# Optimization experiments

Hardware: AMD Instinct MI355X
Metric: run time of the kernel (lower is better)

The kernel has to match this reference:

```python
import jax, jax.numpy as jnp
import numpy as np

N = 250000
E = 8000000
G = 1024  # num graphs
F_IN = 16
H = 9
EPS_BN = 1e-5


def gat_conv(x, edge_index, W, att_src, att_dst, bias):
    # PyG GATConv (heads=1, add_self_loops=True, negative_slope=0.2)
    h = x @ W                               # [N, H]
    src = jnp.concatenate([edge_index[0], jnp.arange(N)])  # self-loops
    dst = jnp.concatenate([edge_index[1], jnp.arange(N)])
    a_src = h @ att_src                     # [N]
    a_dst = h @ att_dst                     # [N]
    e = jax.nn.leaky_relu(a_src[src] + a_dst[dst], 0.2)    # [E+N]
    m = jax.lax.stop_gradient(jax.ops.segment_max(e, dst, num_segments=N))
    ex = jnp.exp(e - m[dst])
    s = jax.ops.segment_sum(ex, dst, num_segments=N)
    alpha = ex / (s[dst] + 1e-16)
    out = jax.ops.segment_sum(h[src] * alpha[:, None], dst, num_segments=N)
    return out + bias


def batch_norm(x, gamma, beta):
    mu = x.mean(0)
    var = x.var(0)  # biased, as PyTorch uses for normalization
    return gamma * (x - mu) * jax.lax.rsqrt(var + EPS_BN) + beta


def setup_inputs() -> dict:
    key = jax.random.key(0)
    ks = jax.random.split(key, 20)
    x = jax.random.normal(ks[0], (N, F_IN), dtype=jnp.float32)
    edge_index = jax.random.randint(ks[1], (2, E), 0, N, dtype=jnp.int64)
    batch = jnp.sort(jax.random.randint(ks[2], (N,), 0, G, dtype=jnp.int64))
    p = {}
    p['W1'] = jax.random.normal(ks[3], (F_IN, H), dtype=jnp.float32) * 0.3
    p['as1'] = jax.random.normal(ks[4], (H,), dtype=jnp.float32) * 0.3
    p['ad1'] = jax.random.normal(ks[5], (H,), dtype=jnp.float32) * 0.3
    p['b1'] = jnp.zeros((H,), dtype=jnp.float32)
    p['g1'] = jnp.ones((H,), dtype=jnp.float32)
    p['be1'] = jnp.zeros((H,), dtype=jnp.float32)
    p['W2'] = jax.random.normal(ks[6], (H, H), dtype=jnp.float32) * 0.3
    p['as2'] = jax.random.normal(ks[7], (H,), dtype=jnp.float32) * 0.3
    p['ad2'] = jax.random.normal(ks[8], (H,), dtype=jnp.float32) * 0.3
    p['b2'] = jnp.zeros((H,), dtype=jnp.float32)
    p['g2'] = jnp.ones((H,), dtype=jnp.float32)
    p['be2'] = jnp.zeros((H,), dtype=jnp.float32)
    for i, (di, do) in enumerate([(H, H), (H, H), (H, H), (H, 1)], start=1):
        p[f'mW{i}'] = jax.random.normal(ks[8 + 2 * i], (di, do), dtype=jnp.float32) * 0.3
        p[f'mb{i}'] = jnp.zeros((do,), dtype=jnp.float32)
    return {'x': x, 'edge_index': edge_index, 'batch': batch, **p}


def reference(x, edge_index, batch, W1, as1, ad1, b1, g1, be1,
              W2, as2, ad2, b2, g2, be2,
              mW1, mb1, mW2, mb2, mW3, mb3, mW4, mb4):
    h = gat_conv(x, edge_index, W1, as1, ad1, b1)
    h = jax.nn.relu(h)
    h = batch_norm(h, g1, be1)
    # dropout is identity at inference
    h = gat_conv(h, edge_index, W2, as2, ad2, b2)
    h = jax.nn.relu(h)
    h = batch_norm(h, g2, be2)
    pooled = jax.ops.segment_sum(h, batch, num_segments=G)  # [G, H]
    o = pooled @ mW1 + mb1
    o = o @ mW2 + mb2
    o = o @ mW3 + mb3
    o = o @ mW4 + mb4
    return o
```

## Files before the change

### kernel.cpp

```cpp
#include <hip/hip_runtime.h>

#define NN 250000
#define NE 8000000
#define NG 1024
#define FIN 16
#define HD 9
#define NSTAGE 64

#define CBIN 1024
#define NPB 245
#define NBK 1024
#define EPB 7813
#define LOFFW 1025
#define SCAP 9216

static __device__ __forceinline__ float lrelu(float v) { return v > 0.f ? v : 0.2f * v; }

static __device__ __forceinline__ unsigned f2bf(float f) {
    unsigned u = __float_as_uint(f);
    return (u + 0x7fffu + ((u >> 16) & 1u)) >> 16;
}
static __device__ __forceinline__ float bf_lo(unsigned u) { return __uint_as_float(u << 16); }
static __device__ __forceinline__ float bf_hi(unsigned u) { return __uint_as_float(u & 0xffff0000u); }

static __device__ __forceinline__ int block_excl_scan(int v, int* total)
{
    int lane = threadIdx.x & 63, wv = threadIdx.x >> 6;
    int ps = v;
#pragma unroll
    for (int o = 1; o < 64; o <<= 1) { int u = __shfl_up(ps, o); if (lane >= o) ps += u; }
    __shared__ int wsum[4];
    if (lane == 63) wsum[wv] = ps;
    __syncthreads();
    int woff = 0;
    for (int w = 0; w < wv; w++) woff += wsum[w];
    if (total) *total = wsum[0] + wsum[1] + wsum[2] + wsum[3];
    __syncthreads();
    return woff + ps - v;
}

__global__ void __launch_bounds__(256) chunk_sort(
    const int* __restrict__ srcs, const int* __restrict__ dsts,
    int* __restrict__ schunk, int* __restrict__ lrow)
{
    __shared__ int hist[CBIN];
    __shared__ int stage[EPB];
    int t = threadIdx.x, b = blockIdx.x;
    int base = b * EPB;
    int end = base + EPB; if (end > NE) end = NE;
    int n = end - base;
    for (int c = t; c < CBIN; c += 256) hist[c] = 0;
    __syncthreads();
    for (int e = base + t; e < end; e += 256)
        atomicAdd(&hist[(unsigned)dsts[e] / NPB], 1);
    __syncthreads();
    int v0 = hist[4*t], v1 = hist[4*t+1], v2 = hist[4*t+2], v3 = hist[4*t+3];
    int ex = block_excl_scan(v0 + v1 + v2 + v3, nullptr);
    int e0 = ex, e1 = ex + v0, e2 = e1 + v1, e3 = e2 + v2;
    hist[4*t] = e0; hist[4*t+1] = e1; hist[4*t+2] = e2; hist[4*t+3] = e3;
    int* lr = lrow + (size_t)b * LOFFW;
    lr[4*t] = e0; lr[4*t+1] = e1; lr[4*t+2] = e2; lr[4*t+3] = e3;
    if (t == 255) lr[CBIN] = n;
    __syncthreads();
    for (int e = base + t; e < end; e += 256) {
        int src = srcs[e], dst = dsts[e];
        int bin = (unsigned)dst / NPB;
        int p = atomicAdd(&hist[bin], 1);
        stage[p] = (src << 8) | (dst - bin * NPB);
    }
    __syncthreads();
    for (int i = t; i < n; i += 256) schunk[base + i] = stage[i];
}

__global__ void __launch_bounds__(256) bin_scan_chunks(
    const int* __restrict__ lrow, int* __restrict__ coffT, int* __restrict__ rstartT,
    int* __restrict__ bintot)
{
    int bin = blockIdx.x, t = threadIdx.x;
    int v[4], st[4]; int sum = 0;
#pragma unroll
    for (int j = 0; j < 4; j++) {
        const int* lr = lrow + (size_t)(4 * t + j) * LOFFW + bin;
        st[j] = lr[0];
        v[j] = lr[1] - lr[0];
        sum += v[j];
    }
    int tot;
    int ex = block_excl_scan(sum, &tot);
    int run = ex;
    int* co = coffT + (size_t)bin * (NBK + 1);
    int* rs = rstartT + (size_t)bin * NBK;
#pragma unroll
    for (int j = 0; j < 4; j++) {
        co[4 * t + j] = run;
        rs[4 * t + j] = st[j];
        run += v[j];
    }
    if (t == 0) bintot[bin] = tot;
    if (t == 255) co[NBK] = run;
}

__global__ void __launch_bounds__(256) bin_scan_bins(const int* __restrict__ bintot, int* __restrict__ binbase)
{
    int t = threadIdx.x;
    int i0 = 4 * t;
    int v0 = bintot[i0], v1 = bintot[i0 + 1], v2 = bintot[i0 + 2], v3 = bintot[i0 + 3];
    int ex = block_excl_scan(v0 + v1 + v2 + v3, nullptr);
    binbase[i0] = ex; binbase[i0 + 1] = ex + v0;
    binbase[i0 + 2] = ex + v0 + v1; binbase[i0 + 3] = ex + v0 + v1 + v2;
    if (t == 255) binbase[CBIN] = ex + v0 + v1 + v2 + v3;
}

__global__ void __launch_bounds__(256) bin_build(
    const int* __restrict__ schunk, const int* __restrict__ coffT, const int* __restrict__ rstartT,
    const int* __restrict__ binbase, int* __restrict__ binned, int* __restrict__ off)
{
    __shared__ int stageA[SCAP];
    __shared__ int stageB[SCAP];
    __shared__ int cntS[256];
    int bin = blockIdx.x, t = threadIdx.x;
    int beg = binbase[bin];
    int n = binbase[bin + 1] - beg; if (n > SCAP) n = SCAP;
    const int* co = coffT + (size_t)bin * (NBK + 1);
    const int* rs = rstartT + (size_t)bin * NBK;
    for (int c = t; c < NBK; c += 256) {
        int o = co[c], len = co[c + 1] - o;
        const int* sp = schunk + (size_t)c * EPB + rs[c];
        for (int j = 0; j < len; j++)
            if (o + j < SCAP) stageA[o + j] = sp[j];
    }
    cntS[t] = 0;
    __syncthreads();
    for (int i = t; i < n; i += 256)
        atomicAdd(&cntS[stageA[i] & 255], 1);
    __syncthreads();
    int ex = block_excl_scan(cntS[t], nullptr);
    int node = bin * NPB + t;
    if (t < NPB && node <= NN) off[node] = beg + ex;
    cntS[t] = ex;
    __syncthreads();
    for (int i = t; i < n; i += 256) {
        int rec = stageA[i];
        int p = atomicAdd(&cntS[rec & 255], 1);
        if (p < SCAP) stageB[p] = rec >> 8;
    }
    __syncthreads();
    for (int i = t; i < n; i += 256) binned[beg + i] = stageB[i];
}

__global__ void __launch_bounds__(256) node_prep1(
    const float* __restrict__ x, const float* __restrict__ W,
    const float* __restrict__ as_, const float* __restrict__ ad_,
    uint2* __restrict__ hq, float* __restrict__ adst,
    float* __restrict__ s, float* __restrict__ acc)
{
    __shared__ float sW[FIN * HD];
    __shared__ float sas[HD], sad[HD];
    for (int t = threadIdx.x; t < FIN * HD; t += 256) sW[t] = W[t];
    if (threadIdx.x < HD) { sas[threadIdx.x] = as_[threadIdx.x]; sad[threadIdx.x] = ad_[threadIdx.x]; }
    __syncthreads();
    int i = blockIdx.x * 256 + threadIdx.x;
    if (i >= NN) return;
    float xi[FIN];
    const float4* xp = reinterpret_cast<const float4*>(x + (size_t)i * FIN);
#pragma unroll
    for (int q = 0; q < 4; q++) { float4 v = xp[q]; xi[4*q] = v.x; xi[4*q+1] = v.y; xi[4*q+2] = v.z; xi[4*q+3] = v.w; }
    float hv[HD];
#pragma unroll
    for (int k = 0; k < HD; k++) {
        float a = 0.f;
#pragma unroll
        for (int j = 0; j < FIN; j++) a = fmaf(xi[j], sW[j * HD + k], a);
        hv[k] = a;
    }
    float sa = 0.f, sd = 0.f;
#pragma unroll
    for (int k = 0; k < HD; k++) { sa = fmaf(hv[k], sas[k], sa); sd = fmaf(hv[k], sad[k], sd); }
    float w = __expf(lrelu(sa + sd));
    adst[i] = sd; s[i] = w;
    uint2* hp = hq + (size_t)i * 3;
    hp[0] = make_uint2(f2bf(hv[0]) | (f2bf(hv[1]) << 16), f2bf(hv[2]) | (f2bf(hv[3]) << 16));
    hp[1] = make_uint2(f2bf(hv[4]) | (f2bf(hv[5]) << 16), f2bf(hv[6]) | (f2bf(hv[7]) << 16));
    hp[2] = make_uint2(f2bf(hv[8]), __float_as_uint(sa));
#pragma unroll
    for (int k = 0; k < HD; k++) acc[(size_t)i*HD+k] = w * hv[k];
}

__global__ void __launch_bounds__(256) node_prep2(
    const float* __restrict__ accin, const float* __restrict__ sin, const float* __restrict__ b,
    const float* __restrict__ sc, const float* __restrict__ sh,
    const float* __restrict__ W, const float* __restrict__ as_, const float* __restrict__ ad_,
    uint2* __restrict__ hq, float* __restrict__ adst,
    float* __restrict__ s, float* __restrict__ acc)
{
    __shared__ float sW[HD * HD];
    __shared__ float sas[HD], sad[HD], ssc[HD], ssh[HD], sb[HD];
    for (int t = threadIdx.x; t < HD * HD; t += 256) sW[t] = W[t];
    if (threadIdx.x < HD) {
        sas[threadIdx.x] = as_[threadIdx.x]; sad[threadIdx.x] = ad_[threadIdx.x];
        ssc[threadIdx.x] = sc[threadIdx.x]; ssh[threadIdx.x] = sh[threadIdx.x];
        sb[threadIdx.x] = b[threadIdx.x];
    }
    __syncthreads();
    int i = blockIdx.x * 256 + threadIdx.x;
    if (i >= NN) return;
    float inv = 1.0f / (sin[i] + 1e-16f);
    float xi[HD];
#pragma unroll
    for (int k = 0; k < HD; k++) {
        float v = fmaf(accin[(size_t)i*HD+k], inv, sb[k]);
        v = v > 0.f ? v : 0.f;
        xi[k] = fmaf(v, ssc[k], ssh[k]);
    }
    float hv[HD];
#pragma unroll
    for (int k = 0; k < HD; k++) {
        float a = 0.f;
#pragma unroll
        for (int j = 0; j < HD; j++) a = fmaf(xi[j], sW[j * HD + k], a);
        hv[k] = a;
    }
    float sa = 0.f, sd = 0.f;
#pragma unroll
    for (int k = 0; k < HD; k++) { sa = fmaf(hv[k], sas[k], sa); sd = fmaf(hv[k], sad[k], sd); }
    float w = __expf(lrelu(sa + sd));
    adst[i] = sd; s[i] = w;
    uint2* hp = hq + (size_t)i * 3;
    hp[0] = make_uint2(f2bf(hv[0]) | (f2bf(hv[1]) << 16), f2bf(hv[2]) | (f2bf(hv[3]) << 16));
    hp[1] = make_uint2(f2bf(hv[4]) | (f2bf(hv[5]) << 16), f2bf(hv[6]) | (f2bf(hv[7]) << 16));
    hp[2] = make_uint2(f2bf(hv[8]), __float_as_uint(sa));
#pragma unroll
    for (int k = 0; k < HD; k++) acc[(size_t)i*HD+k] = w * hv[k];
}

#define ACCUM(w, A, B, C) \
    a[0] = fmaf(w, bf_lo(A.x), a[0]); a[1] = fmaf(w, bf_hi(A.x), a[1]); \
    a[2] = fmaf(w, bf_lo(A.y), a[2]); a[3] = fmaf(w, bf_hi(A.y), a[3]); \
    a[4] = fmaf(w, bf_lo(B.x), a[4]); a[5] = fmaf(w, bf_hi(B.x), a[5]); \
    a[6] = fmaf(w, bf_lo(B.y), a[6]); a[7] = fmaf(w, bf_hi(B.y), a[7]); \
    a[8] = fmaf(w, bf_lo(C.x), a[8]);

__global__ void __launch_bounds__(256) gat_gather(
    const int* __restrict__ off, const int* __restrict__ esrc,
    const uint2* __restrict__ hq, const float* __restrict__ adst,
    float* __restrict__ s, float* __restrict__ acc)
{
    int gidx = blockIdx.x * 32 + (threadIdx.x >> 3);
    int lane = threadIdx.x & 7;
    if (gidx >= NN) return;
    int beg = off[gidx], end = off[gidx + 1];
    float ad = adst[gidx];
    float wsum = 0.f;
    float a[HD];
#pragma unroll
    for (int k = 0; k < HD; k++) a[k] = 0.f;
    int e = beg + lane;
    for (; e + 8 < end; e += 16) {
        int s0 = esrc[e], s1 = esrc[e + 8];
        const uint2* p0 = hq + (size_t)s0 * 3;
        const uint2* p1 = hq + (size_t)s1 * 3;
        uint2 A0 = p0[0], B0 = p0[1], C0 = p0[2];
        uint2 A1 = p1[0], B1 = p1[1], C1 = p1[2];
        float w0 = __expf(lrelu(__uint_as_float(C0.y) + ad));
        float w1 = __expf(lrelu(__uint_as_float(C1.y) + ad));
        wsum += w0 + w1;
        ACCUM(w0, A0, B0, C0);
        ACCUM(w1, A1, B1, C1);
    }
    if (e < end) {
        int s0 = esrc[e];
        const uint2* p0 = hq + (size_t)s0 * 3;
        uint2 A0 = p0[0], B0 = p0[1], C0 = p0[2];
        float w0 = __expf(lrelu(__uint_as_float(C0.y) + ad));
        wsum += w0;
        ACCUM(w0, A0, B0, C0);
    }
#pragma unroll
    for (int o = 1; o < 8; o <<= 1) {
        wsum += __shfl_xor(wsum, o);
#pragma unroll
        for (int k = 0; k < HD; k++) a[k] += __shfl_xor(a[k], o);
    }
    if (lane == 0) {
        s[gidx] += wsum;
        float* ap = acc + (size_t)gidx * HD;
#pragma unroll
        for (int k = 0; k < HD; k++) ap[k] += a[k];
    }
}

__global__ void __launch_bounds__(256) node_finish1(
    const float* __restrict__ acc, const float* __restrict__ s, const float* __restrict__ b,
    float* __restrict__ stage)
{
    int i = blockIdx.x * 256 + threadIdx.x;
    bool act = i < NN;
    float inv = act ? 1.0f / (s[i] + 1e-16f) : 0.f;
    float y[HD];
#pragma unroll
    for (int k = 0; k < HD; k++) {
        float v = act ? fmaf(acc[(size_t)i*HD+k], inv, __ldg(&b[k])) : 0.f;
        y[k] = v > 0.f ? v : 0.f;
    }
    __shared__ float red[4][2 * HD];
    int lane = threadIdx.x & 63, wv = threadIdx.x >> 6;
#pragma unroll
    for (int k = 0; k < HD; k++) {
        float sm = y[k], sq = y[k] * y[k];
#pragma unroll
        for (int o = 32; o > 0; o >>= 1) { sm += __shfl_down(sm, o); sq += __shfl_down(sq, o); }
        if (lane == 0) { red[wv][k] = sm; red[wv][HD + k] = sq; }
    }
    __syncthreads();
    int t = threadIdx.x;
    if (t < 2 * HD) {
        float v = red[0][t] + red[1][t] + red[2][t] + red[3][t];
        atomicAdd(&stage[(blockIdx.x & (NSTAGE - 1)) * 2 * HD + t], v);
    }
}

__global__ void __launch_bounds__(256) node_finish2(
    const float* __restrict__ acc, const float* __restrict__ s, const float* __restrict__ b,
    const int* __restrict__ batch,
    float* __restrict__ stage,
    float* __restrict__ pool, float* __restrict__ cnt)
{
    int i = blockIdx.x * 256 + threadIdx.x;
    bool act = i < NN;
    float inv = act ? 1.0f / (s[i] + 1e-16f) : 0.f;
    float y[HD];
#pragma unroll
    for (int k = 0; k < HD; k++) {
        float v = act ? fmaf(acc[(size_t)i*HD+k], inv, __ldg(&b[k])) : 0.f;
        y[k] = v > 0.f ? v : 0.f;
    }
    __shared__ float red[4][2 * HD];
    int lane = threadIdx.x & 63, wv = threadIdx.x >> 6;
#pragma unroll
    for (int k = 0; k < HD; k++) {
        float sm = y[k], sq = y[k] * y[k];
#pragma unroll
        for (int o = 32; o > 0; o >>= 1) { sm += __shfl_down(sm, o); sq += __shfl_down(sq, o); }
        if (lane == 0) { red[wv][k] = sm; red[wv][HD + k] = sq; }
    }
    __syncthreads();
    int t = threadIdx.x;
    if (t < 2 * HD) {
        float v = red[0][t] + red[1][t] + red[2][t] + red[3][t];
        atomicAdd(&stage[(blockIdx.x & (NSTAGE - 1)) * 2 * HD + t], v);
    }
    int g = act ? batch[i] : -1;
    unsigned long long alive = __ballot(g >= 0);
    while (alive) {
        int leader = (int)__builtin_ctzll(alive);
        int g0 = __shfl(g, leader);
        bool mine = (g == g0);
#pragma unroll
        for (int k = 0; k < HD; k++) {
            float v = mine ? y[k] : 0.f;
#pragma unroll
            for (int o = 32; o > 0; o >>= 1) v += __shfl_xor(v, o);
            if (lane == leader) atomicAdd(&pool[g0 * HD + k], v);
        }
        float c = mine ? 1.f : 0.f;
#pragma unroll
        for (int o = 32; o > 0; o >>= 1) c += __shfl_xor(c, o);
        if (lane == leader) atomicAdd(&cnt[g0], c);
        alive &= ~__ballot(mine);
    }
}

__global__ void bn_finalize(const float* __restrict__ stage,
                            const float* __restrict__ gamma, const float* __restrict__ beta,
                            float* __restrict__ scale, float* __restrict__ shift)
{
    __shared__ float tot[2 * HD];
    int t = threadIdx.x;
    if (t < 2 * HD) {
        float v = 0.f;
        for (int j = 0; j < NSTAGE; j++) v += stage[j * 2 * HD + t];
        tot[t] = v;
    }
    __syncthreads();
    if (t < HD) {
        float mu = tot[t] * (1.0f / NN);
        float var = tot[HD + t] * (1.0f / NN) - mu * mu;
        float rstd = rsqrtf(var + 1e-5f);
        float sc = gamma[t] * rstd;
        scale[t] = sc;
        shift[t] = beta[t] - mu * sc;
    }
}

__global__ void __launch_bounds__(256) final_mlp(
    const float* __restrict__ pool, const float* __restrict__ cnt,
    const float* __restrict__ sc, const float* __restrict__ sh,
    const float* __restrict__ mW1, const float* __restrict__ mb1,
    const float* __restrict__ mW2, const float* __restrict__ mb2,
    const float* __restrict__ mW3, const float* __restrict__ mb3,
    const float* __restrict__ mW4, const float* __restrict__ mb4,
    float* __restrict__ out)
{
    __shared__ float w1[81], w2[81], w3[81], bb1[9], bb2[9], bb3[9], w4[9], ssc[9], ssh[9];
    int t = threadIdx.x;
    if (t < 81) { w1[t] = mW1[t]; w2[t] = mW2[t]; w3[t] = mW3[t]; }
    if (t < 9) {
        bb1[t] = mb1[t]; bb2[t] = mb2[t]; bb3[t] = mb3[t];
        w4[t] = mW4[t]; ssc[t] = sc[t]; ssh[t] = sh[t];
    }
    __syncthreads();
    int g = blockIdx.x * 256 + t;
    if (g >= NG) return;
    float c = cnt[g];
    float p[9], q[9];
#pragma unroll
    for (int k = 0; k < 9; k++) p[k] = fmaf(ssc[k], pool[g * 9 + k], ssh[k] * c);
#pragma unroll
    for (int k = 0; k < 9; k++) {
        float a = bb1[k];
#pragma unroll
        for (int j = 0; j < 9; j++) a = fmaf(p[j], w1[j * 9 + k], a);
        q[k] = a;
    }
#pragma unroll
    for (int k = 0; k < 9; k++) {
        float a = bb2[k];
#pragma unroll
        for (int j = 0; j < 9; j++) a = fmaf(q[j], w2[j * 9 + k], a);
        p[k] = a;
    }
#pragma unroll
    for (int k = 0; k < 9; k++) {
        float a = bb3[k];
#pragma unroll
        for (int j = 0; j < 9; j++) a = fmaf(p[j], w3[j * 9 + k], a);
        q[k] = a;
    }
    float o = mb4[0];
#pragma unroll
    for (int j = 0; j < 9; j++) o = fmaf(q[j], w4[j], o);
    out[g] = o;
}

extern "C" void kernel_launch(void* const* d_in, const int* in_sizes, int n_in,
                              void* d_out, int out_size, void* d_ws, size_t ws_size,
                              hipStream_t stream)
{
    const float* x   = (const float*)d_in[0];
    const int*   ei  = (const int*)d_in[1];
    const int*   bat = (const int*)d_in[2];
    const float* W1  = (const float*)d_in[3];
    const float* as1 = (const float*)d_in[4];
    const float* ad1 = (const float*)d_in[5];
    const float* b1  = (const float*)d_in[6];
    const float* g1  = (const float*)d_in[7];
    const float* be1 = (const float*)d_in[8];
    const float* W2  = (const float*)d_in[9];
    const float* as2 = (const float*)d_in[10];
    const float* ad2 = (const float*)d_in[11];
    const float* b2  = (const float*)d_in[12];
    const float* g2  = (const float*)d_in[13];
    const float* be2 = (const float*)d_in[14];
    const float* mW1 = (const float*)d_in[15];
    const float* mb1 = (const float*)d_in[16];
    const float* mW2 = (const float*)d_in[17];
    const float* mb2 = (const float*)d_in[18];
    const float* mW3 = (const float*)d_in[19];
    const float* mb3 = (const float*)d_in[20];
    const float* mW4 = (const float*)d_in[21];
    const float* mb4 = (const float*)d_in[22];
    float* out = (float*)d_out;

    float* ws   = (float*)d_ws;
    float* zb   = ws;
    float* stg1 = zb;
    float* stg2 = stg1 + NSTAGE * 2 * HD;
    float* pool = stg2 + NSTAGE * 2 * HD;
    float* cnt  = pool + (size_t)NG * HD;
    float* sc1  = cnt + NG;
    float* sh1  = sc1 + HD;
    float* sc2  = sh1 + HD;
    float* sh2  = sc2 + HD;
    int*   off    = (int*)(sh2 + HD);
    int*   binned = off + (NN + 1);
    int*   uni    = binned + NE;
    int*   schunk = uni;
    uint2* hq     = (uint2*)uni;
    float* adst   = (float*)uni + (size_t)NN * 6;
    float* s      = adst + NN;
    float* acc    = s + NN;
    int*   lrow    = uni + NE;
    int*   coffT   = lrow + (size_t)NBK * LOFFW;
    int*   rstartT = coffT + (size_t)CBIN * (NBK + 1);
    int*   bintot  = rstartT + (size_t)CBIN * NBK;
    int*   binbase = bintot + CBIN;

    size_t zbytes = (size_t)(2 * NSTAGE * 2 * HD + NG * HD + NG + 4 * HD) * sizeof(float);
    hipMemsetAsync(zb, 0, zbytes, stream);

    const int* srcs = ei;
    const int* dsts = ei + NE;
    int nb  = (NN + 255) / 256;
    int ngb = (NN + 31) / 32;

    chunk_sort<<<NBK, 256, 0, stream>>>(srcs, dsts, schunk, lrow);
    bin_scan_chunks<<<CBIN, 256, 0, stream>>>(lrow, coffT, rstartT, bintot);
    bin_scan_bins<<<1, 256, 0, stream>>>(bintot, binbase);
    bin_build<<<CBIN, 256, 0, stream>>>(schunk, coffT, rstartT, binbase, binned, off);

    node_prep1<<<nb, 256, 0, stream>>>(x, W1, as1, ad1, hq, adst, s, acc);
    gat_gather<<<ngb, 256, 0, stream>>>(off, binned, hq, adst, s, acc);
    node_finish1<<<nb, 256, 0, stream>>>(acc, s, b1, stg1);
    bn_finalize<<<1, 64, 0, stream>>>(stg1, g1, be1, sc1, sh1);

    node_prep2<<<nb, 256, 0, stream>>>(acc, s, b1, sc1, sh1, W2, as2, ad2, hq, adst, s, acc);
    gat_gather<<<ngb, 256, 0, stream>>>(off, binned, hq, adst, s, acc);
    node_finish2<<<nb, 256, 0, stream>>>(acc, s, b2, bat, stg2, pool, cnt);
    bn_finalize<<<1, 64, 0, stream>>>(stg2, g2, be2, sc2, sh2);

    final_mlp<<<(NG + 255) / 256, 256, 0, stream>>>(pool, cnt, sc2, sh2,
                                                    mW1, mb1, mW2, mb2, mW3, mb3, mW4, mb4, out);
}
```

Measured before the change: 343.4 us.

## Split gather edges by source half to keep feature reads L2-resident

The edge binning now tags each edge with whether its source lies in the lower or upper half of the nodes. Each destination's edges are sorted into two sub-segments, and per-node offsets are stored in a doubled offset array. The GAT gather then runs twice per layer, each pass reading only one half of the bf16 feature table, so the randomly accessed working set is halved and more likely to stay in L2. In exchange it adds an extra kernel launch per layer and reads and writes the per-node accumulators and offsets twice.

```diff
diff --git a/kernel.cpp b/kernel.cpp
--- a/kernel.cpp
+++ b/kernel.cpp
@@ -13,6 +13,8 @@
 #define EPB 7813
 #define LOFFW 1025
 #define SCAP 9216
+#define NHALF 125000
+#define NKEY 512
 
 static __device__ __forceinline__ float lrelu(float v) { return v > 0.f ? v : 0.2f * v; }
 
@@ -65,8 +67,9 @@
     for (int e = base + t; e < end; e += 256) {
         int src = srcs[e], dst = dsts[e];
         int bin = (unsigned)dst / NPB;
+        int key = (dst - bin * NPB) * 2 + (src >= NHALF ? 1 : 0);
         int p = atomicAdd(&hist[bin], 1);
-        stage[p] = (src << 8) | (dst - bin * NPB);
+        stage[p] = (src << 9) | key;
     }
     __syncthreads();
     for (int i = t; i < n; i += 256) schunk[base + i] = stage[i];
@@ -113,11 +116,11 @@
 
 __global__ void __launch_bounds__(256) bin_build(
     const int* __restrict__ schunk, const int* __restrict__ coffT, const int* __restrict__ rstartT,
-    const int* __restrict__ binbase, int* __restrict__ binned, int* __restrict__ off)
+    const int* __restrict__ binbase, int* __restrict__ binned, int* __restrict__ off2)
 {
     __shared__ int stageA[SCAP];
     __shared__ int stageB[SCAP];
-    __shared__ int cntS[256];
+    __shared__ int cntS[NKEY];
     int bin = blockIdx.x, t = threadIdx.x;
     int beg = binbase[bin];
     int n = binbase[bin + 1] - beg; if (n > SCAP) n = SCAP;
@@ -129,20 +132,26 @@
         for (int j = 0; j < len; j++)
             if (o + j < SCAP) stageA[o + j] = sp[j];
     }
-    cntS[t] = 0;
+    cntS[t] = 0; cntS[t + 256] = 0;
     __syncthreads();
     for (int i = t; i < n; i += 256)
-        atomicAdd(&cntS[stageA[i] & 255], 1);
-    __syncthreads();
-    int ex = block_excl_scan(cntS[t], nullptr);
-    int node = bin * NPB + t;
-    if (t < NPB && node <= NN) off[node] = beg + ex;
-    cntS[t] = ex;
+        atomicAdd(&cntS[stageA[i] & (NKEY - 1)], 1);
+    __syncthreads();
+    int v0 = cntS[2 * t], v1 = cntS[2 * t + 1];
+    int ex = block_excl_scan(v0 + v1, nullptr);
+    {
+        long long node0 = (long long)bin * NPB + t;
+        if (t < NPB && node0 <= NN) {
+            off2[2 * node0]     = beg + ex;
+            if (node0 < NN) off2[2 * node0 + 1] = beg + ex + v0;
+        }
+    }
+    cntS[2 * t] = ex; cntS[2 * t + 1] = ex + v0;
     __syncthreads();
     for (int i = t; i < n; i += 256) {
         int rec = stageA[i];
-        int p = atomicAdd(&cntS[rec & 255], 1);
-        if (p < SCAP) stageB[p] = rec >> 8;
+        int p = atomicAdd(&cntS[rec & (NKEY - 1)], 1);
+        if (p < SCAP) stageB[p] = rec >> 9;
     }
     __syncthreads();
     for (int i = t; i < n; i += 256) binned[beg + i] = stageB[i];
@@ -241,14 +250,14 @@
     a[8] = fmaf(w, bf_lo(C.x), a[8]);
 
 __global__ void __launch_bounds__(256) gat_gather(
-    const int* __restrict__ off, const int* __restrict__ esrc,
+    const int* __restrict__ off2, const int* __restrict__ esrc,
     const uint2* __restrict__ hq, const float* __restrict__ adst,
-    float* __restrict__ s, float* __restrict__ acc)
+    float* __restrict__ s, float* __restrict__ acc, int half)
 {
     int gidx = blockIdx.x * 32 + (threadIdx.x >> 3);
     int lane = threadIdx.x & 7;
     if (gidx >= NN) return;
-    int beg = off[gidx], end = off[gidx + 1];
+    int beg = off2[2 * gidx + half], end = off2[2 * gidx + half + 1];
     float ad = adst[gidx];
     float wsum = 0.f;
     float a[HD];
@@ -481,8 +490,8 @@
     float* sh1  = sc1 + HD;
     float* sc2  = sh1 + HD;
     float* sh2  = sc2 + HD;
-    int*   off    = (int*)(sh2 + HD);
-    int*   binned = off + (NN + 1);
+    int*   off2   = (int*)(sh2 + HD);
+    int*   binned = off2 + (2 * NN + 1);
     int*   uni    = binned + NE;
     int*   schunk = uni;
     uint2* hq     = (uint2*)uni;
@@ -506,15 +515,17 @@
     chunk_sort<<<NBK, 256, 0, stream>>>(srcs, dsts, schunk, lrow);
     bin_scan_chunks<<<CBIN, 256, 0, stream>>>(lrow, coffT, rstartT, bintot);
     bin_scan_bins<<<1, 256, 0, stream>>>(bintot, binbase);
-    bin_build<<<CBIN, 256, 0, stream>>>(schunk, coffT, rstartT, binbase, binned, off);
+    bin_build<<<CBIN, 256, 0, stream>>>(schunk, coffT, rstartT, binbase, binned, off2);
 
     node_prep1<<<nb, 256, 0, stream>>>(x, W1, as1, ad1, hq, adst, s, acc);
-    gat_gather<<<ngb, 256, 0, stream>>>(off, binned, hq, adst, s, acc);
+    gat_gather<<<ngb, 256, 0, stream>>>(off2, binned, hq, adst, s, acc, 0);
+    gat_gather<<<ngb, 256, 0, stream>>>(off2, binned, hq, adst, s, acc, 1);
     node_finish1<<<nb, 256, 0, stream>>>(acc, s, b1, stg1);
     bn_finalize<<<1, 64, 0, stream>>>(stg1, g1, be1, sc1, sh1);
 
     node_prep2<<<nb, 256, 0, stream>>>(acc, s, b1, sc1, sh1, W2, as2, ad2, hq, adst, s, acc);
-    gat_gather<<<ngb, 256, 0, stream>>>(off, binned, hq, adst, s, acc);
+    gat_gather<<<ngb, 256, 0, stream>>>(off2, binned, hq, adst, s, acc, 0);
+    gat_gather<<<ngb, 256, 0, stream>>>(off2, binned, hq, adst, s, acc, 1);
     node_finish2<<<nb, 256, 0, stream>>>(acc, s, b2, bat, stg2, pool, cnt);
     bn_finalize<<<1, 64, 0, stream>>>(stg2, g2, be2, sc2, sh2);
 
```

New measurement: 318.4 us. 1.08x faster.
